# Optimization experiments

Hardware: AMD Instinct MI355X
Metric: run time of the kernel (lower is better)

Reference implementation:

```python
import jax, jax.numpy as jnp
import numpy as np

D_MODEL = 1024
D_ATTN = 1024
N_HEADS = 16
D_FF = 4096
EPS = 1e-6


def _ln(x, gamma, beta):
    # Matches the custom LayerNorm: (x - mean) / (std + eps), std = sqrt(biased var)
    mean = jnp.mean(x, axis=-1, keepdims=True)
    std = jnp.sqrt(jnp.mean((x - mean) ** 2, axis=-1, keepdims=True))
    return gamma * ((x - mean) / (std + EPS)) + beta


def setup_inputs() -> dict:
    key = jax.random.key(0)
    ks = jax.random.split(key, 16)
    s = 0.02
    d, da, dff = D_MODEL, D_ATTN, D_FF
    inp = {
        "x": jax.random.normal(ks[0], (1, 2048, d), dtype=jnp.float32),
        "g1": jnp.ones((d,), jnp.float32),
        "beta1": jnp.zeros((d,), jnp.float32),
        "W_in": jax.random.normal(ks[1], (d, da), jnp.float32) * s,
        "b_in": jnp.zeros((da,), jnp.float32),
        "Wq": jax.random.normal(ks[2], (da, da), jnp.float32) * s,
        "bq": jnp.zeros((da,), jnp.float32),
        "Wk": jax.random.normal(ks[3], (da, da), jnp.float32) * s,
        "bk": jnp.zeros((da,), jnp.float32),
        "Wv": jax.random.normal(ks[4], (da, da), jnp.float32) * s,
        "bv": jnp.zeros((da,), jnp.float32),
        "Wo": jax.random.normal(ks[5], (da, da), jnp.float32) * s,
        "bo": jnp.zeros((da,), jnp.float32),
        "W2": jax.random.normal(ks[6], (da, d), jnp.float32) * s,
        "b2": jnp.zeros((d,), jnp.float32),
        "g2": jnp.ones((d,), jnp.float32),
        "beta2": jnp.zeros((d,), jnp.float32),
        "Wf1": jax.random.normal(ks[7], (d, dff), jnp.float32) * s,
        "bf1": jnp.zeros((dff,), jnp.float32),
        "Wf2": jax.random.normal(ks[8], (dff, d), jnp.float32) * s,
        "bf2": jnp.zeros((d,), jnp.float32),
    }
    return inp


def reference(x, g1, beta1, W_in, b_in, Wq, bq, Wk, bk, Wv, bv, Wo, bo,
              W2, b2, g2, beta2, Wf1, bf1, Wf2, bf2):
    B, S, _ = x.shape
    H, dk = N_HEADS, D_ATTN // N_HEADS

    norm_x = _ln(x, g1, beta1)
    h = norm_x @ W_in + b_in                      # [B,S,d_attn]

    def split_heads(t):
        return t.reshape(B, S, H, dk).transpose(0, 2, 1, 3)  # [B,H,S,dk]

    q = split_heads(h @ Wq + bq)
    k = split_heads(h @ Wk + bk)
    v = split_heads(h @ Wv + bv)

    scores = jnp.einsum("bhqd,bhkd->bhqk", q, k) / jnp.sqrt(jnp.float32(dk))
    causal = jnp.tril(jnp.ones((S, S), bool))[None, None]
    scores = jnp.where(causal, scores, -jnp.inf)
    attn_weights = jax.nn.softmax(scores, axis=-1)            # [B,H,S,S]
    ctx = jnp.einsum("bhqk,bhkd->bhqd", attn_weights, v)
    ctx = ctx.transpose(0, 2, 1, 3).reshape(B, S, D_ATTN)
    mha_out = ctx @ Wo + bo

    part1 = x + (mha_out @ W2 + b2)
    norm2 = _ln(part1, g2, beta2)
    ff = jnp.maximum(norm2 @ Wf1 + bf1, 0.0) @ Wf2 + bf2
    out = norm2 + ff
    return out, attn_weights
```

## Files before the change

### kernel.cpp

```cpp
#include <hip/hip_runtime.h>
#include <hip/hip_bf16.h>
#include <cstdint>

#define S_LEN 2048
#define D_MOD 1024
#define N_HEADS 16
#define DK 64
#define D_FF 4096

typedef __bf16 bf16x8 __attribute__((ext_vector_type(8)));
typedef float f32x4 __attribute__((ext_vector_type(4)));

#define MFMA16(a, b, c) __builtin_amdgcn_mfma_f32_16x16x32_bf16((a), (b), (c), 0, 0, 0)

__device__ inline unsigned pack_bf16x2(float a, float b)
{
    unsigned short ua = __builtin_bit_cast(unsigned short, (__bf16)a);
    unsigned short ub = __builtin_bit_cast(unsigned short, (__bf16)b);
    return (unsigned)ua | ((unsigned)ub << 16);
}

__device__ inline void gload16(const void* g, void* l)
{
    __builtin_amdgcn_global_load_lds(
        (const __attribute__((address_space(1))) unsigned int*)g,
        (__attribute__((address_space(3))) unsigned int*)l, 16, 0, 0);
}

template<int BN, bool RELU, bool RES, bool RES2, bool WF32, bool WBF16, bool WVT>
__device__ __forceinline__
void gemm_dev(const __bf16* __restrict__ A, const __bf16* __restrict__ BT,
              const float* __restrict__ bias, const float* __restrict__ res,
              const float* __restrict__ res2,
              float* __restrict__ Cf, __bf16* __restrict__ Cb,
              __bf16* __restrict__ vt,
              int N, int Kst, int Klp, int bx, int by,
              uint4* As, uint4* Bs)
{
    constexpr int NFRAG = BN / 32;
    const int tid = threadIdx.x;
    const int lane = tid & 63;
    const int w = tid >> 6;
    const int lrow = lane & 15;
    const int g = lane >> 4;
    const int bm = by * 128;
    const int bn = bx * BN;
    const int wrow = (w >> 1) * 64;
    const int wcol = (w & 1) * (BN / 2);

    f32x4 acc[4][NFRAG];
    for (int m = 0; m < 4; m++)
        for (int n = 0; n < NFRAG; n++)
            acc[m][n] = (f32x4){0.f, 0.f, 0.f, 0.f};

    const int srow = tid >> 3;
    const int sc = tid & 7;
    const __bf16* Ag = A + (size_t)(bm + srow) * Kst + sc * 8;
    const __bf16* Bg = BT + (size_t)(bn + srow) * Kst + sc * 8;

    for (int kt = 0; kt < Klp; kt += 64) {
        __syncthreads();
        #pragma unroll
        for (int p = 0; p < 4; p++)
            gload16(Ag + (size_t)(p * 32) * Kst + kt, &As[(srow + p * 32) * 8 + sc]);
        #pragma unroll
        for (int p = 0; p < NFRAG; p++)
            gload16(Bg + (size_t)(p * 32) * Kst + kt, &Bs[(srow + p * 32) * 8 + sc]);
        asm volatile("s_waitcnt vmcnt(0)" ::: "memory");
        __syncthreads();
        #pragma unroll
        for (int kk = 0; kk < 2; kk++) {
            bf16x8 af[4], bfr[NFRAG];
            int c = kk * 4 + g;
            #pragma unroll
            for (int m = 0; m < 4; m++)
                af[m] = __builtin_bit_cast(bf16x8, As[(wrow + m * 16 + lrow) * 8 + c]);
            #pragma unroll
            for (int n = 0; n < NFRAG; n++)
                bfr[n] = __builtin_bit_cast(bf16x8, Bs[(wcol + n * 16 + lrow) * 8 + c]);
            #pragma unroll
            for (int m = 0; m < 4; m++)
                #pragma unroll
                for (int n = 0; n < NFRAG; n++)
                    acc[m][n] = MFMA16(af[m], bfr[n], acc[m][n]);
        }
    }

    for (int n = 0; n < NFRAG; n++) {
        int col = bn + wcol + n * 16 + lrow;
        float bval = bias ? bias[col] : 0.f;
        for (int m = 0; m < 4; m++) {
            int row0 = bm + wrow + m * 16 + g * 4;
            float vv[4];
            for (int r = 0; r < 4; r++) {
                int row = row0 + r;
                float v = acc[m][n][r] + bval;
                if (RELU) v = fmaxf(v, 0.f);
                if (RES) v += res[(size_t)row * N + col];
                if (RES2) v += res2[(size_t)row * N + col];
                vv[r] = v;
                if (WF32) Cf[(size_t)row * N + col] = v;
                if (WBF16) Cb[(size_t)row * N + col] = (__bf16)v;
            }
            if (WVT && col >= 2048) {
                uint2 pk;
                pk.x = pack_bf16x2(vv[0], vv[1]);
                pk.y = pack_bf16x2(vv[2], vv[3]);
                *(uint2*)(vt + (size_t)(col - 2048) * S_LEN + row0) = pk;
            }
        }
    }
}

__device__ __forceinline__
void ln_row(int row, const float* __restrict__ x, const float* __restrict__ gamma,
            const float* __restrict__ beta, __bf16* __restrict__ outb,
            float* __restrict__ outf, float* red)
{
    int tid = threadIdx.x;
    const float4 v = ((const float4*)(x + (size_t)row * D_MOD))[tid];
    float s = v.x + v.y + v.z + v.w;
    float sq = v.x * v.x + v.y * v.y + v.z * v.z + v.w * v.w;
    for (int off = 32; off; off >>= 1) {
        s += __shfl_down(s, off);
        sq += __shfl_down(sq, off);
    }
    int wid = tid >> 6;
    if ((tid & 63) == 0) { red[wid] = s; red[wid + 4] = sq; }
    __syncthreads();
    s = red[0] + red[1] + red[2] + red[3];
    sq = red[4] + red[5] + red[6] + red[7];
    float mean = s * (1.f / D_MOD);
    float var = fmaxf(sq * (1.f / D_MOD) - mean * mean, 0.f);
    float inv = 1.f / (sqrtf(var) + 1e-6f);
    float4 gv = ((const float4*)gamma)[tid];
    float4 bv = ((const float4*)beta)[tid];
    float y0 = gv.x * ((v.x - mean) * inv) + bv.x;
    float y1 = gv.y * ((v.y - mean) * inv) + bv.y;
    float y2 = gv.z * ((v.z - mean) * inv) + bv.z;
    float y3 = gv.w * ((v.w - mean) * inv) + bv.w;
    uint2 pk;
    pk.x = pack_bf16x2(y0, y1);
    pk.y = pack_bf16x2(y2, y3);
    ((uint2*)(outb + (size_t)row * D_MOD))[tid] = pk;
    if (outf) {
        float4 o = {y0, y1, y2, y3};
        ((float4*)(outf + (size_t)row * D_MOD))[tid] = o;
    }
}

__device__ __forceinline__
void pwrite_tile(const __bf16* __restrict__ qkv, const float* __restrict__ Obuf,
                 float* __restrict__ P, int h, int qt, int kt)
{
    const int tid = threadIdx.x;
    const int lane = tid & 63;
    const int w = tid >> 6;
    const int lrow = lane & 15;
    const int g = lane >> 4;
    const float c1 = 0.18033688f;
    const __bf16* ksec = qkv + 1024;
    const size_t Pb = (size_t)h * S_LEN * S_LEN;

    bf16x8 qfr[2][2];
    #pragma unroll
    for (int qq = 0; qq < 2; qq++)
        #pragma unroll
        for (int kk = 0; kk < 2; kk++)
            qfr[qq][kk] = *(const bf16x8*)(qkv +
                (size_t)(qt * 128 + w * 32 + qq * 16 + lrow) * 3072 + h * DK + kk * 32 + g * 8);

    f32x4 acc[2][8];
    #pragma unroll
    for (int qq = 0; qq < 2; qq++)
        #pragma unroll
        for (int mf = 0; mf < 8; mf++) acc[qq][mf] = (f32x4){0.f, 0.f, 0.f, 0.f};
    #pragma unroll
    for (int kk = 0; kk < 2; kk++) {
        #pragma unroll
        for (int mf = 0; mf < 8; mf++) {
            bf16x8 kf = *(const bf16x8*)(ksec +
                (size_t)(kt * 128 + mf * 16 + lrow) * 3072 + h * DK + kk * 32 + g * 8);
            acc[0][mf] = MFMA16(kf, qfr[0][kk], acc[0][mf]);
            acc[1][mf] = MFMA16(kf, qfr[1][kk], acc[1][mf]);
        }
    }

    #pragma unroll
    for (int qq = 0; qq < 2; qq++) {
        int q = qt * 128 + w * 32 + qq * 16 + lrow;
        float offv = Obuf[h * S_LEN + q];
        float* prow = P + Pb + (size_t)q * S_LEN;
        if (kt == qt) {
            #pragma unroll
            for (int mf = 0; mf < 8; mf++) {
                int kvb = kt * 128 + mf * 16 + g * 4;
                f32x4 st;
                st[0] = (kvb + 0 <= q) ? exp2f(acc[qq][mf][0] * c1 + offv) : 0.f;
                st[1] = (kvb + 1 <= q) ? exp2f(acc[qq][mf][1] * c1 + offv) : 0.f;
                st[2] = (kvb + 2 <= q) ? exp2f(acc[qq][mf][2] * c1 + offv) : 0.f;
                st[3] = (kvb + 3 <= q) ? exp2f(acc[qq][mf][3] * c1 + offv) : 0.f;
                __builtin_nontemporal_store(st, (f32x4*)(prow + kvb));
            }
        } else {
            #pragma unroll
            for (int mf = 0; mf < 8; mf++) {
                int kvb = kt * 128 + mf * 16 + g * 4;
                f32x4 st;
                st[0] = exp2f(acc[qq][mf][0] * c1 + offv);
                st[1] = exp2f(acc[qq][mf][1] * c1 + offv);
                st[2] = exp2f(acc[qq][mf][2] * c1 + offv);
                st[3] = exp2f(acc[qq][mf][3] * c1 + offv);
                __builtin_nontemporal_store(st, (f32x4*)(prow + kvb));
            }
        }
    }
}

__device__ __forceinline__
void zfill_tile(float* __restrict__ P, int zid)
{
    int tid = threadIdx.x;
    int h = zid / 120;
    int pr = zid - h * 120;
    int qt = 0, acc = 0;
    while (pr >= acc + 15 - qt) { acc += 15 - qt; qt++; }
    int kt = qt + 1 + (pr - acc);
    f32x4 z = {0.f, 0.f, 0.f, 0.f};
    float* base = P + (size_t)h * S_LEN * S_LEN + (size_t)(qt * 128) * S_LEN + kt * 128;
    #pragma unroll
    for (int i = 0; i < 16; i++) {
        int idx = i * 256 + tid;
        int row = idx >> 5, c = idx & 31;
        __builtin_nontemporal_store(z, (f32x4*)(base + (size_t)row * S_LEN + c * 4));
    }
}

__global__ __launch_bounds__(256)
void prep1(const float* __restrict__ Wq, const float* __restrict__ Wk,
           const float* __restrict__ Wv, const float* __restrict__ W2,
           const float* __restrict__ Wf1, const float* __restrict__ Wf2,
           const float* __restrict__ W_in, const float* __restrict__ Wo,
           const float* __restrict__ b_in, const float* __restrict__ bo,
           __bf16* __restrict__ WqkvT, __bf16* __restrict__ W2T,
           __bf16* __restrict__ Wf1T, __bf16* __restrict__ Wf2T,
           __bf16* __restrict__ Win_b, __bf16* __restrict__ Wo_b,
           float* __restrict__ part)
{
    __shared__ float tile[32][33];
    int id = blockIdx.x;
    int tid = threadIdx.x;
    if (id < 12288) {
        const float* W; __bf16* WT; int K, N, n0, k0;
        if (id < 4096) {
            int m = id >> 10; id &= 1023;
            K = 1024; N = 1024;
            n0 = (id & 31) * 32; k0 = (id >> 5) * 32;
            W = m == 0 ? Wq : (m == 1 ? Wk : (m == 2 ? Wv : W2));
            WT = m == 3 ? W2T : WqkvT + (size_t)m * 1024 * 1024;
        } else if (id < 8192) {
            id -= 4096;
            K = 1024; N = 4096;
            n0 = (id & 127) * 32; k0 = (id >> 7) * 32;
            W = Wf1; WT = Wf1T;
        } else {
            id -= 8192;
            K = 4096; N = 1024;
            n0 = (id & 31) * 32; k0 = (id >> 5) * 32;
            W = Wf2; WT = Wf2T;
        }
        int tx = tid & 31, ty = tid >> 5;
        for (int i = 0; i < 4; i++)
            tile[ty + i * 8][tx] = W[(size_t)(k0 + ty + i * 8) * N + n0 + tx];
        __syncthreads();
        for (int i = 0; i < 4; i++)
            WT[(size_t)(n0 + ty + i * 8) * K + k0 + tx] = (__bf16)tile[tx][ty + i * 8];
        return;
    }
    id -= 12288;
    if (id < 2048) {
        const float* W = id < 1024 ? W_in : Wo;
        __bf16* o = id < 1024 ? Win_b : Wo_b;
        int i = (id & 1023) * 256 + tid;
        float4 v = ((const float4*)W)[i];
        uint2 pk;
        pk.x = pack_bf16x2(v.x, v.y);
        pk.y = pack_bf16x2(v.z, v.w);
        ((uint2*)o)[i] = pk;
        return;
    }
    id -= 2048;
    {
        int n = (id & 15) * 256 + tid;
        int kc = id >> 4;
        int sel = n >> 10, col = n & 1023;
        const float* W = sel == 0 ? Wq : (sel == 1 ? Wk : (sel == 2 ? Wv : W2));
        const float* src = sel < 3 ? b_in : bo;
        float s = 0.f;
        for (int k = kc * 128; k < kc * 128 + 128; k++)
            s += src[k] * W[(size_t)k * 1024 + col];
        part[kc * 4096 + n] = s;
    }
}

__global__ __launch_bounds__(256, 2)
void prep2(const __bf16* __restrict__ WqkvT, const __bf16* __restrict__ Win_b,
           __bf16* __restrict__ WqkvCT,
           const __bf16* __restrict__ W2T, const __bf16* __restrict__ Wo_b,
           __bf16* __restrict__ WcombT,
           const float* __restrict__ part,
           const float* __restrict__ bq, const float* __restrict__ bk,
           const float* __restrict__ bv, const float* __restrict__ b2,
           float* __restrict__ bqkv, float* __restrict__ bcomb,
           const float* __restrict__ x, const float* __restrict__ g1,
           const float* __restrict__ beta1, __bf16* __restrict__ xn_b)
{
    __shared__ uint4 As[128 * 8];
    __shared__ uint4 Bs[64 * 8];
    int id = blockIdx.x;
    int tid = threadIdx.x;
    if (id < 384) {
        gemm_dev<64, false, false, false, false, true, false>(
            WqkvT, Win_b, nullptr, nullptr, nullptr, nullptr, WqkvCT, nullptr,
            1024, 1024, 1024, id & 15, id >> 4, As, Bs);
        return;
    }
    id -= 384;
    if (id < 128) {
        gemm_dev<64, false, false, false, false, true, false>(
            W2T, Wo_b, nullptr, nullptr, nullptr, nullptr, WcombT, nullptr,
            1024, 1024, 1024, id & 15, id >> 4, As, Bs);
        return;
    }
    id -= 128;
    if (id < 16) {
        int n = id * 256 + tid;
        int sel = n >> 10, col = n & 1023;
        float s = sel == 0 ? bq[col] : (sel == 1 ? bk[col] : (sel == 2 ? bv[col] : b2[col]));
        for (int kc = 0; kc < 8; kc++) s += part[kc * 4096 + n];
        if (n < 3072) bqkv[n] = s; else bcomb[col] = s;
        return;
    }
    id -= 16;
    ln_row(id, x, g1, beta1, xn_b, nullptr, (float*)As);
}

__global__ __launch_bounds__(256, 2)
void qkv_zf(const __bf16* __restrict__ xn_b, const __bf16* __restrict__ WqkvCT,
            const float* __restrict__ bqkv, __bf16* __restrict__ qkv_b,
            __bf16* __restrict__ vt, float* __restrict__ P)
{
    __shared__ uint4 As[128 * 8];
    __shared__ uint4 Bs[128 * 8];
    if (blockIdx.x < 384) {
        int bid = blockIdx.x;
        gemm_dev<128, false, false, false, false, true, true>(
            xn_b, WqkvCT, bqkv, nullptr, nullptr, nullptr, qkv_b, vt,
            3072, 1024, 1024, bid % 24, bid / 24, As, Bs);
        return;
    }
    zfill_tile(P, blockIdx.x - 384);
}

template<int BN, bool RELU, bool RES, bool RES2, bool WF32, bool WBF16>
__global__ __launch_bounds__(256, 2)
void gemm_kernel(const __bf16* __restrict__ A, const __bf16* __restrict__ BT,
                 const float* __restrict__ bias, const float* __restrict__ res,
                 const float* __restrict__ res2,
                 float* __restrict__ Cf, __bf16* __restrict__ Cb,
                 int N, int Kst, int Klp)
{
    __shared__ uint4 As[128 * 8];
    __shared__ uint4 Bs[BN * 8];
    gemm_dev<BN, RELU, RES, RES2, WF32, WBF16, false>(
        A, BT, bias, res, res2, Cf, Cb, nullptr, N, Kst, Klp,
        blockIdx.x, blockIdx.y, As, Bs);
}

__global__ __launch_bounds__(256)
void ln_kernel(const float* __restrict__ x, const float* __restrict__ gamma,
               const float* __restrict__ beta, __bf16* __restrict__ outb,
               float* __restrict__ outf)
{
    __shared__ float red[8];
    ln_row(blockIdx.x, x, gamma, beta, outb, outf, red);
}

__global__ __launch_bounds__(256, 2)
void attn_flash(const __bf16* __restrict__ qkv, const __bf16* __restrict__ vt,
                float* __restrict__ Obuf, __bf16* __restrict__ ctx,
                float* __restrict__ P)
{
    __shared__ char Ks[2][16384];
    __shared__ char Vs[2][16384];
    __shared__ char Plds[4][4096];
    const int tid = threadIdx.x;

    if (blockIdx.x >= 512) {
        zfill_tile(P, 960 + (int)blockIdx.x - 512);
        return;
    }

    const int lane = tid & 63;
    const int w = tid >> 6;
    const int lrow = lane & 15;
    const int g = lane >> 4;
    const int h = blockIdx.x & 15;
    const int b = 31 - ((int)blockIdx.x >> 4);
    const int qg = b * 64 + w * 16 + lrow;
    const int ntiles = (b >> 1) + 1;
    const float c1 = 0.18033688f;
    const __bf16* ksec = qkv + 1024;
    char* plB = Plds[w];

    bf16x8 qf[2];
    qf[0] = *(const bf16x8*)(qkv + (size_t)qg * 3072 + h * DK + g * 8);
    qf[1] = *(const bf16x8*)(qkv + (size_t)qg * 3072 + h * DK + 32 + g * 8);

    float m2 = -1e30f, l = 0.f;
    f32x4 acc2[4];
    #pragma unroll
    for (int i = 0; i < 4; i++) acc2[i] = (f32x4){0.f, 0.f, 0.f, 0.f};

    const int sKrow = (w << 3) + (lane >> 3);
    const int sKch = lane & 7;
    const int sVrow = (w << 2) + (lane >> 4);
    const int sVch = lane & 15;

    auto stage = [&](int kt, int tb) {
        char* KsW = Ks[tb] + w * 1024;
        char* VsW = Vs[tb] + w * 1024;
        #pragma unroll
        for (int p = 0; p < 4; p++) {
            int row = sKrow + p * 32;
            int ch = sKch ^ (row & 7);
            gload16(ksec + (size_t)(kt * 128 + row) * 3072 + h * DK + ch * 8,
                    KsW + p * 4096 + lane * 16);
        }
        #pragma unroll
        for (int p = 0; p < 4; p++) {
            int row = sVrow + p * 16;
            int ch = sVch ^ (row & 7);
            gload16(vt + (size_t)(h * DK + row) * S_LEN + kt * 128 + ch * 8,
                    VsW + p * 4096 + lane * 16);
        }
    };

    stage(0, 0);

    for (int kt = 0; kt < ntiles; kt++) {
        const int cur = kt & 1;
        if (kt + 1 < ntiles) {
            stage(kt + 1, cur ^ 1);
            asm volatile("s_waitcnt vmcnt(8)" ::: "memory");
        } else {
            asm volatile("s_waitcnt vmcnt(0)" ::: "memory");
        }
        __syncthreads();

        const char* Ksb = Ks[cur];
        const char* Vsb = Vs[cur];

        f32x4 acc[8];
        #pragma unroll
        for (int mf = 0; mf < 8; mf++) acc[mf] = (f32x4){0.f, 0.f, 0.f, 0.f};
        #pragma unroll
        for (int kk = 0; kk < 2; kk++)
            #pragma unroll
            for (int mf = 0; mf < 8; mf++) {
                int row = mf * 16 + lrow;
                bf16x8 kf = *(const bf16x8*)(Ksb + row * 128 + (((kk * 4 + g) ^ (row & 7)) << 4));
                acc[mf] = MFMA16(kf, qf[kk], acc[mf]);
            }

        float s[8][4];
        float tmx = -1e30f;
        const bool lastT = (kt == ntiles - 1);
        #pragma unroll
        for (int mf = 0; mf < 8; mf++) {
            int kvb = kt * 128 + mf * 16 + g * 4;
            #pragma unroll
            for (int r = 0; r < 4; r++) {
                float sv = acc[mf][r] * c1;
                if (lastT) sv = (kvb + r <= qg) ? sv : -1e30f;
                s[mf][r] = sv;
                tmx = fmaxf(tmx, sv);
            }
        }
        if (!__all((int)(tmx <= m2 + 6.f))) {
            float tm = fmaxf(tmx, __shfl_xor(tmx, 16));
            tm = fmaxf(tm, __shfl_xor(tm, 32));
            float nm = fmaxf(m2, tm);
            float sc = exp2f(m2 - nm);
            l *= sc;
            #pragma unroll
            for (int md = 0; md < 4; md++) acc2[md] *= sc;
            m2 = nm;
        }
        float sum = 0.f;
        #pragma unroll
        for (int mf = 0; mf < 8; mf++) {
            float p0 = exp2f(s[mf][0] - m2);
            float p1 = exp2f(s[mf][1] - m2);
            float p2 = exp2f(s[mf][2] - m2);
            float p3 = exp2f(s[mf][3] - m2);
            sum += (p0 + p1) + (p2 + p3);
            uint2 pk;
            pk.x = pack_bf16x2(p0, p1);
            pk.y = pack_bf16x2(p2, p3);
            *(uint2*)(plB + ((lrow * 256 + mf * 32 + g * 8) ^ ((lrow & 7) << 4))) = pk;
        }
        l += sum;

        #pragma unroll
        for (int ks = 0; ks < 4; ks++) {
            bf16x8 pf = *(bf16x8*)(plB + ((lrow * 256 + ks * 64 + g * 16) ^ ((lrow & 7) << 4)));
            #pragma unroll
            for (int md = 0; md < 4; md++) {
                int row = md * 16 + lrow;
                bf16x8 vf = *(const bf16x8*)(Vsb + row * 256 + (((ks * 4 + g) ^ (row & 7)) << 4));
                acc2[md] = MFMA16(vf, pf, acc2[md]);
            }
        }
        __syncthreads();
    }

    l += __shfl_xor(l, 16);
    l += __shfl_xor(l, 32);
    float li = 1.f / l;
    if (lane < 16)
        Obuf[h * S_LEN + qg] = -m2 - log2f(l);
    #pragma unroll
    for (int md = 0; md < 4; md++) {
        uint2 pk;
        pk.x = pack_bf16x2(acc2[md][0] * li, acc2[md][1] * li);
        pk.y = pack_bf16x2(acc2[md][2] * li, acc2[md][3] * li);
        *(uint2*)(ctx + (size_t)qg * D_MOD + h * DK + md * 16 + g * 4) = pk;
    }
}

__global__ __launch_bounds__(256)
void ff1_pwrite(const __bf16* __restrict__ A, const __bf16* __restrict__ BT,
                const float* __restrict__ bias, __bf16* __restrict__ Cb,
                const __bf16* __restrict__ qkv, const float* __restrict__ Obuf,
                float* __restrict__ P)
{
    __shared__ uint4 As[128 * 8];
    __shared__ uint4 Bs[128 * 8];
    if (blockIdx.x < 512) {
        int bid = blockIdx.x;
        gemm_dev<128, true, false, false, false, true, false>(
            A, BT, bias, nullptr, nullptr, nullptr, Cb, nullptr,
            D_FF, 1024, 1024, bid & 31, bid >> 5, As, Bs);
        return;
    }
    int idp = blockIdx.x - 512;
    int h = idp / 136;
    int tt = idp - h * 136;
    int qt = 0;
    while (tt > qt) { tt -= qt + 1; qt++; }
    pwrite_tile(qkv, Obuf, P, h, qt, tt);
}

__global__ __launch_bounds__(256)
void ff2_pwrite(const __bf16* __restrict__ ff1_b, const __bf16* __restrict__ Wf2T,
                float* __restrict__ partA, float* __restrict__ partB,
                const __bf16* __restrict__ qkv, const float* __restrict__ Obuf,
                float* __restrict__ P)
{
    __shared__ uint4 As[128 * 8];
    __shared__ uint4 Bs[64 * 8];
    if (blockIdx.x < 512) {
        int half = blockIdx.x >> 8;
        int b2 = blockIdx.x & 255;
        const __bf16* Ah = ff1_b + half * 2048;
        const __bf16* Bh = Wf2T + half * 2048;
        float* Cf = half ? partB : partA;
        gemm_dev<64, false, false, false, true, false, false>(
            Ah, Bh, nullptr, nullptr, nullptr, Cf, nullptr, nullptr,
            1024, 4096, 2048, b2 & 15, b2 >> 4, As, Bs);
        return;
    }
    int idp = blockIdx.x - 512;
    int h = 8 + idp / 136;
    int tt = idp - (idp / 136) * 136;
    int qt = 0;
    while (tt > qt) { tt -= qt + 1; qt++; }
    pwrite_tile(qkv, Obuf, P, h, qt, tt);
}

__global__ __launch_bounds__(256)
void ff2_reduce(const float* __restrict__ partA, const float* __restrict__ partB,
                const float* __restrict__ norm2f, const float* __restrict__ bf2,
                float* __restrict__ outp)
{
    int idx = blockIdx.x * 256 + threadIdx.x;
    int col = (idx * 4) & 1023;
    f32x4 a = *(const f32x4*)(partA + (size_t)idx * 4);
    f32x4 b = *(const f32x4*)(partB + (size_t)idx * 4);
    f32x4 n = *(const f32x4*)(norm2f + (size_t)idx * 4);
    f32x4 bb = *(const f32x4*)(bf2 + col);
    f32x4 o = a + b + n + bb;
    *(f32x4*)(outp + (size_t)idx * 4) = o;
}

extern "C" void kernel_launch(void* const* d_in, const int* in_sizes, int n_in,
                              void* d_out, int out_size, void* d_ws, size_t ws_size,
                              hipStream_t stream)
{
    const float* x     = (const float*)d_in[0];
    const float* g1    = (const float*)d_in[1];
    const float* beta1 = (const float*)d_in[2];
    const float* W_in  = (const float*)d_in[3];
    const float* b_in  = (const float*)d_in[4];
    const float* Wq    = (const float*)d_in[5];
    const float* bq    = (const float*)d_in[6];
    const float* Wk    = (const float*)d_in[7];
    const float* bk    = (const float*)d_in[8];
    const float* Wv    = (const float*)d_in[9];
    const float* bv    = (const float*)d_in[10];
    const float* Wo    = (const float*)d_in[11];
    const float* bo    = (const float*)d_in[12];
    const float* W2    = (const float*)d_in[13];
    const float* b2    = (const float*)d_in[14];
    const float* g2    = (const float*)d_in[15];
    const float* beta2 = (const float*)d_in[16];
    const float* Wf1   = (const float*)d_in[17];
    const float* bf1   = (const float*)d_in[18];
    const float* Wf2   = (const float*)d_in[19];
    const float* bf2   = (const float*)d_in[20];

    float* outp = (float*)d_out;
    float* Pout = outp + (size_t)S_LEN * D_MOD;

    char* p = (char*)d_ws;
    auto alloc = [&](size_t b) -> void* {
        void* r = (void*)p;
        p += (b + 255) & ~(size_t)255;
        return r;
    };
    __bf16* WqkvT    = (__bf16*)alloc((size_t)3072 * 1024 * 2);
    __bf16* W2T      = (__bf16*)alloc((size_t)1024 * 1024 * 2);
    __bf16* Wf1T     = (__bf16*)alloc((size_t)D_FF * D_MOD * 2);
    __bf16* Wf2T     = (__bf16*)alloc((size_t)D_MOD * D_FF * 2);
    __bf16* WqkvCT   = (__bf16*)alloc((size_t)3072 * 1024 * 2);
    __bf16* WcombT   = (__bf16*)alloc((size_t)1024 * 1024 * 2);
    float*  bqkv     = (float*)alloc((size_t)3072 * 4);
    float*  bcomb    = (float*)alloc((size_t)1024 * 4);
    float*  biaspart = (float*)alloc((size_t)8 * 4096 * 4);
    __bf16* xn_b     = (__bf16*)alloc((size_t)S_LEN * D_MOD * 2);
    __bf16* qkv_b    = (__bf16*)alloc((size_t)S_LEN * 3072 * 2);
    __bf16* VT       = (__bf16*)alloc((size_t)N_HEADS * DK * S_LEN * 2);
    __bf16* ctx_b    = (__bf16*)alloc((size_t)S_LEN * D_MOD * 2);
    float*  part1f   = (float*)alloc((size_t)S_LEN * D_MOD * 4);
    float*  norm2f   = (float*)alloc((size_t)S_LEN * D_MOD * 4);
    __bf16* norm2b   = (__bf16*)alloc((size_t)S_LEN * D_MOD * 2);
    __bf16* ff1_b    = (__bf16*)alloc((size_t)S_LEN * D_FF * 2);
    float*  Obuf     = (float*)alloc((size_t)N_HEADS * S_LEN * 4);
    float*  ffpartB  = (float*)alloc((size_t)S_LEN * D_MOD * 4);
    __bf16* Win_b   = (__bf16*)part1f;
    __bf16* Wo_b    = (__bf16*)norm2f;
    float*  ffpartA = part1f;

    dim3 blk(256);

    prep1<<<dim3(14464), blk, 0, stream>>>(Wq, Wk, Wv, W2, Wf1, Wf2, W_in, Wo,
                                           b_in, bo, WqkvT, W2T, Wf1T, Wf2T,
                                           Win_b, Wo_b, biaspart);

    prep2<<<dim3(2576), blk, 0, stream>>>(WqkvT, Win_b, WqkvCT, W2T, Wo_b, WcombT,
                                          biaspart, bq, bk, bv, b2, bqkv, bcomb,
                                          x, g1, beta1, xn_b);

    qkv_zf<<<dim3(384 + 960), blk, 0, stream>>>(xn_b, WqkvCT, bqkv, qkv_b, VT, Pout);

    attn_flash<<<dim3(512 + 960), blk, 0, stream>>>(qkv_b, VT, Obuf, ctx_b, Pout);

    gemm_kernel<64, false, true, false, true, false><<<dim3(16, 16), blk, 0, stream>>>(
        ctx_b, WcombT, bcomb, x, nullptr, part1f, nullptr, 1024, 1024, 1024);

    ln_kernel<<<S_LEN, blk, 0, stream>>>(part1f, g2, beta2, norm2b, norm2f);

    ff1_pwrite<<<dim3(512 + 1088), blk, 0, stream>>>(
        norm2b, Wf1T, bf1, ff1_b, qkv_b, Obuf, Pout);

    ff2_pwrite<<<dim3(512 + 1088), blk, 0, stream>>>(
        ff1_b, Wf2T, ffpartA, ffpartB, qkv_b, Obuf, Pout);

    ff2_reduce<<<dim3(2048), blk, 0, stream>>>(ffpartA, ffpartB, norm2f, bf2, outp);
}
```

Baseline: 260.2 us.

## Double-buffer GEMM LDS tiles and split-K the output projection with fused LN

The shared GEMM device routine now double-buffers its A/B LDS tiles, issuing the next K-tile's global-to-LDS loads before computing on the current one, with partial vmcnt waits. The ctx×Wcomb projection becomes a split-K launch of 512 blocks writing two fp32 partials. A new LN kernel sums the partials, residual and bias before normalizing, replacing the old GEMM epilogue and the separate LN read. LDS per block doubles and occupancy hints are added to the FF kernels, which may lower occupancy and costs an extra 8MB partial buffer round trip.

Result: slower. 267.5 us (+2.8%).

```diff
diff --git a/kernel.cpp b/kernel.cpp
--- a/kernel.cpp
+++ b/kernel.cpp
@@ -58,32 +58,51 @@
     const __bf16* Ag = A + (size_t)(bm + srow) * Kst + sc * 8;
     const __bf16* Bg = BT + (size_t)(bn + srow) * Kst + sc * 8;
 
-    for (int kt = 0; kt < Klp; kt += 64) {
+    auto stage = [&](int kt, int tb) {
+        uint4* Ad = As + tb * 128 * 8;
+        uint4* Bd = Bs + tb * BN * 8;
+        #pragma unroll
+        for (int p = 0; p < 4; p++)
+            gload16(Ag + (size_t)(p * 32) * Kst + kt, &Ad[(srow + p * 32) * 8 + sc]);
+        #pragma unroll
+        for (int p = 0; p < NFRAG; p++)
+            gload16(Bg + (size_t)(p * 32) * Kst + kt, &Bd[(srow + p * 32) * 8 + sc]);
+    };
+
+    stage(0, 0);
+
+    int it = 0;
+    for (int kt = 0; kt < Klp; kt += 64, ++it) {
+        const int cur = it & 1;
+        if (kt + 64 < Klp) {
+            stage(kt + 64, cur ^ 1);
+            if constexpr (NFRAG == 4)
+                asm volatile("s_waitcnt vmcnt(8)" ::: "memory");
+            else
+                asm volatile("s_waitcnt vmcnt(6)" ::: "memory");
+        } else {
+            asm volatile("s_waitcnt vmcnt(0)" ::: "memory");
+        }
         __syncthreads();
-        #pragma unroll
-        for (int p = 0; p < 4; p++)
-            gload16(Ag + (size_t)(p * 32) * Kst + kt, &As[(srow + p * 32) * 8 + sc]);
-        #pragma unroll
-        for (int p = 0; p < NFRAG; p++)
-            gload16(Bg + (size_t)(p * 32) * Kst + kt, &Bs[(srow + p * 32) * 8 + sc]);
-        asm volatile("s_waitcnt vmcnt(0)" ::: "memory");
-        __syncthreads();
+        const uint4* Ab = As + cur * 128 * 8;
+        const uint4* Bb = Bs + cur * BN * 8;
         #pragma unroll
         for (int kk = 0; kk < 2; kk++) {
             bf16x8 af[4], bfr[NFRAG];
             int c = kk * 4 + g;
             #pragma unroll
             for (int m = 0; m < 4; m++)
-                af[m] = __builtin_bit_cast(bf16x8, As[(wrow + m * 16 + lrow) * 8 + c]);
+                af[m] = __builtin_bit_cast(bf16x8, Ab[(wrow + m * 16 + lrow) * 8 + c]);
             #pragma unroll
             for (int n = 0; n < NFRAG; n++)
-                bfr[n] = __builtin_bit_cast(bf16x8, Bs[(wcol + n * 16 + lrow) * 8 + c]);
+                bfr[n] = __builtin_bit_cast(bf16x8, Bb[(wcol + n * 16 + lrow) * 8 + c]);
             #pragma unroll
             for (int m = 0; m < 4; m++)
                 #pragma unroll
                 for (int n = 0; n < NFRAG; n++)
                     acc[m][n] = MFMA16(af[m], bfr[n], acc[m][n]);
         }
+        __syncthreads();
     }
 
     for (int n = 0; n < NFRAG; n++) {
@@ -113,12 +132,11 @@
 }
 
 __device__ __forceinline__
-void ln_row(int row, const float* __restrict__ x, const float* __restrict__ gamma,
-            const float* __restrict__ beta, __bf16* __restrict__ outb,
-            float* __restrict__ outf, float* red)
+void ln_row_v(int row, float4 v, const float* __restrict__ gamma,
+              const float* __restrict__ beta, __bf16* __restrict__ outb,
+              float* __restrict__ outf, float* red)
 {
     int tid = threadIdx.x;
-    const float4 v = ((const float4*)(x + (size_t)row * D_MOD))[tid];
     float s = v.x + v.y + v.z + v.w;
     float sq = v.x * v.x + v.y * v.y + v.z * v.z + v.w * v.w;
     for (int off = 32; off; off >>= 1) {
@@ -150,6 +168,15 @@
 }
 
 __device__ __forceinline__
+void ln_row(int row, const float* __restrict__ x, const float* __restrict__ gamma,
+            const float* __restrict__ beta, __bf16* __restrict__ outb,
+            float* __restrict__ outf, float* red)
+{
+    float4 v = ((const float4*)(x + (size_t)row * D_MOD))[threadIdx.x];
+    ln_row_v(row, v, gamma, beta, outb, outf, red);
+}
+
+__device__ __forceinline__
 void pwrite_tile(const __bf16* __restrict__ qkv, const float* __restrict__ Obuf,
                  float* __restrict__ P, int h, int qt, int kt)
 {
@@ -315,8 +342,8 @@
            const float* __restrict__ x, const float* __restrict__ g1,
            const float* __restrict__ beta1, __bf16* __restrict__ xn_b)
 {
-    __shared__ uint4 As[128 * 8];
-    __shared__ uint4 Bs[64 * 8];
+    __shared__ uint4 As[2 * 128 * 8];
+    __shared__ uint4 Bs[2 * 64 * 8];
     int id = blockIdx.x;
     int tid = threadIdx.x;
     if (id < 384) {
@@ -350,8 +377,8 @@
             const float* __restrict__ bqkv, __bf16* __restrict__ qkv_b,
             __bf16* __restrict__ vt, float* __restrict__ P)
 {
-    __shared__ uint4 As[128 * 8];
-    __shared__ uint4 Bs[128 * 8];
+    __shared__ uint4 As[2 * 128 * 8];
+    __shared__ uint4 Bs[2 * 128 * 8];
     if (blockIdx.x < 384) {
         int bid = blockIdx.x;
         gemm_dev<128, false, false, false, false, true, true>(
@@ -362,28 +389,41 @@
     zfill_tile(P, blockIdx.x - 384);
 }
 
-template<int BN, bool RELU, bool RES, bool RES2, bool WF32, bool WBF16>
 __global__ __launch_bounds__(256, 2)
-void gemm_kernel(const __bf16* __restrict__ A, const __bf16* __restrict__ BT,
-                 const float* __restrict__ bias, const float* __restrict__ res,
-                 const float* __restrict__ res2,
-                 float* __restrict__ Cf, __bf16* __restrict__ Cb,
-                 int N, int Kst, int Klp)
-{
-    __shared__ uint4 As[128 * 8];
-    __shared__ uint4 Bs[BN * 8];
-    gemm_dev<BN, RELU, RES, RES2, WF32, WBF16, false>(
-        A, BT, bias, res, res2, Cf, Cb, nullptr, N, Kst, Klp,
-        blockIdx.x, blockIdx.y, As, Bs);
+void part1_split(const __bf16* __restrict__ ctx_b, const __bf16* __restrict__ WcombT,
+                 float* __restrict__ pA, float* __restrict__ pB)
+{
+    __shared__ uint4 As[2 * 128 * 8];
+    __shared__ uint4 Bs[2 * 64 * 8];
+    int half = blockIdx.x >> 8;
+    int b2 = blockIdx.x & 255;
+    const __bf16* Ah = ctx_b + half * 512;
+    const __bf16* Bh = WcombT + half * 512;
+    float* Cf = half ? pB : pA;
+    gemm_dev<64, false, false, false, true, false, false>(
+        Ah, Bh, nullptr, nullptr, nullptr, Cf, nullptr, nullptr,
+        1024, 1024, 512, b2 & 15, b2 >> 4, As, Bs);
 }
 
 __global__ __launch_bounds__(256)
-void ln_kernel(const float* __restrict__ x, const float* __restrict__ gamma,
-               const float* __restrict__ beta, __bf16* __restrict__ outb,
-               float* __restrict__ outf)
+void ln2_fused(const float* __restrict__ pA, const float* __restrict__ pB,
+               const float* __restrict__ x, const float* __restrict__ bcomb,
+               const float* __restrict__ gamma, const float* __restrict__ beta,
+               __bf16* __restrict__ outb, float* __restrict__ outf)
 {
     __shared__ float red[8];
-    ln_row(blockIdx.x, x, gamma, beta, outb, outf, red);
+    int row = blockIdx.x;
+    int tid = threadIdx.x;
+    float4 a = ((const float4*)(pA + (size_t)row * D_MOD))[tid];
+    float4 b = ((const float4*)(pB + (size_t)row * D_MOD))[tid];
+    float4 xv = ((const float4*)(x + (size_t)row * D_MOD))[tid];
+    float4 bc = ((const float4*)bcomb)[tid];
+    float4 v;
+    v.x = a.x + b.x + xv.x + bc.x;
+    v.y = a.y + b.y + xv.y + bc.y;
+    v.z = a.z + b.z + xv.z + bc.z;
+    v.w = a.w + b.w + xv.w + bc.w;
+    ln_row_v(row, v, gamma, beta, outb, outf, red);
 }
 
 __global__ __launch_bounds__(256, 2)
@@ -539,14 +579,14 @@
     }
 }
 
-__global__ __launch_bounds__(256)
+__global__ __launch_bounds__(256, 2)
 void ff1_pwrite(const __bf16* __restrict__ A, const __bf16* __restrict__ BT,
                 const float* __restrict__ bias, __bf16* __restrict__ Cb,
                 const __bf16* __restrict__ qkv, const float* __restrict__ Obuf,
                 float* __restrict__ P)
 {
-    __shared__ uint4 As[128 * 8];
-    __shared__ uint4 Bs[128 * 8];
+    __shared__ uint4 As[2 * 128 * 8];
+    __shared__ uint4 Bs[2 * 128 * 8];
     if (blockIdx.x < 512) {
         int bid = blockIdx.x;
         gemm_dev<128, true, false, false, false, true, false>(
@@ -562,14 +602,14 @@
     pwrite_tile(qkv, Obuf, P, h, qt, tt);
 }
 
-__global__ __launch_bounds__(256)
+__global__ __launch_bounds__(256, 2)
 void ff2_pwrite(const __bf16* __restrict__ ff1_b, const __bf16* __restrict__ Wf2T,
                 float* __restrict__ partA, float* __restrict__ partB,
                 const __bf16* __restrict__ qkv, const float* __restrict__ Obuf,
                 float* __restrict__ P)
 {
-    __shared__ uint4 As[128 * 8];
-    __shared__ uint4 Bs[64 * 8];
+    __shared__ uint4 As[2 * 128 * 8];
+    __shared__ uint4 Bs[2 * 64 * 8];
     if (blockIdx.x < 512) {
         int half = blockIdx.x >> 8;
         int b2 = blockIdx.x & 255;
@@ -653,6 +693,7 @@
     __bf16* VT       = (__bf16*)alloc((size_t)N_HEADS * DK * S_LEN * 2);
     __bf16* ctx_b    = (__bf16*)alloc((size_t)S_LEN * D_MOD * 2);
     float*  part1f   = (float*)alloc((size_t)S_LEN * D_MOD * 4);
+    float*  p1B      = (float*)alloc((size_t)S_LEN * D_MOD * 4);
     float*  norm2f   = (float*)alloc((size_t)S_LEN * D_MOD * 4);
     __bf16* norm2b   = (__bf16*)alloc((size_t)S_LEN * D_MOD * 2);
     __bf16* ff1_b    = (__bf16*)alloc((size_t)S_LEN * D_FF * 2);
@@ -676,10 +717,10 @@
 
     attn_flash<<<dim3(512 + 960), blk, 0, stream>>>(qkv_b, VT, Obuf, ctx_b, Pout);
 
-    gemm_kernel<64, false, true, false, true, false><<<dim3(16, 16), blk, 0, stream>>>(
-        ctx_b, WcombT, bcomb, x, nullptr, part1f, nullptr, 1024, 1024, 1024);
-
-    ln_kernel<<<S_LEN, blk, 0, stream>>>(part1f, g2, beta2, norm2b, norm2f);
+    part1_split<<<dim3(512), blk, 0, stream>>>(ctx_b, WcombT, part1f, p1B);
+
+    ln2_fused<<<S_LEN, blk, 0, stream>>>(part1f, p1B, x, bcomb, g2, beta2,
+                                         norm2b, norm2f);
 
     ff1_pwrite<<<dim3(512 + 1088), blk, 0, stream>>>(
         norm2b, Wf1T, bf1, ff1_b, qkv_b, Obuf, Pout);
```
